# Kernel optimization log

Measured on AMD Instinct MI355X. Metric: run time of the kernel, lower is better.

## Reference

```python
import jax, jax.numpy as jnp
import numpy as np

THRESH = 0.3  # ternary threshold on |W|/mean(|W|)

def ternary_quantize(W):
    # scale = mean(|W|) clamped; q in {-1,0,+1} * scale
    scale = jnp.maximum(jnp.mean(jnp.abs(W)), 1e-8)
    ws = W / scale
    q = jnp.where(ws > THRESH, 1.0, jnp.where(ws < -THRESH, -1.0, 0.0))
    return q * scale

def quantize_activations(y):
    # per-token (last-dim) max-abs int8-style fake quant
    m = jnp.maximum(jnp.max(jnp.abs(y), axis=-1, keepdims=True), 1e-5)
    scale = 127.0 / m
    return jnp.round(jnp.clip(y * scale, -127.0, 127.0)) / scale

def setup_inputs() -> dict:
    key = jax.random.key(0)
    k1, k2, k3, k4, k5 = jax.random.split(key, 5)
    N, D_IN, D_OUT = 16384, 2048, 2048
    x = jax.random.normal(k1, (N, D_IN), dtype=jnp.float32)
    W = jax.random.normal(k2, (D_OUT, D_IN), dtype=jnp.float32) * 0.02
    b = jax.random.normal(k3, (D_OUT,), dtype=jnp.float32) * 0.02
    We = jax.random.normal(k4, (D_OUT, D_IN), dtype=jnp.float32) * 0.02
    be = jax.random.normal(k5, (D_OUT,), dtype=jnp.float32) * 0.02
    return {"x": x, "W": W, "b": b, "We": We, "be": be}

def reference(x, W, b, We, be):
    chain = jax.nn.relu(x @ ternary_quantize(W).T + b)  # [N, D_OUT]
    encoded = x @ We.T + be                              # [N, D_OUT]
    return quantize_activations(chain + encoded)
```

## Files before the change

kernel.cpp:

```cpp
#include <hip/hip_runtime.h>
#include <hip/hip_bf16.h>
#include <math.h>

typedef __bf16 bf16;
typedef __bf16 bf16x8 __attribute__((ext_vector_type(8)));
typedef float  f32x4  __attribute__((ext_vector_type(4)));
typedef unsigned int u32;

#define NROWS 16384
#define KDIM  2048
#define NCOLS 2048

#define OFF_XBF   0
#define OFF_Q     67108864
#define OFF_EBF   75497472
#define OFF_PART  83886080
#define OFF_SCALE 83894272

__device__ __forceinline__ void gload16(const bf16* g, bf16* l) {
    __builtin_amdgcn_global_load_lds(
        (const __attribute__((address_space(1))) u32*)g,
        (__attribute__((address_space(3))) u32*)l,
        16, 0, 0);
}

__device__ __forceinline__ void BAR() {
    asm volatile("" ::: "memory");
    __builtin_amdgcn_s_barrier();
    asm volatile("" ::: "memory");
}

__global__ void k_rowsum_absW(const float* __restrict__ W, float* __restrict__ partials) {
    int row = blockIdx.x;
    int t = threadIdx.x;
    const float4* wr = (const float4*)(W + (size_t)row * KDIM);
    float4 a = wr[t * 2];
    float4 b = wr[t * 2 + 1];
    float s = fabsf(a.x) + fabsf(a.y) + fabsf(a.z) + fabsf(a.w)
            + fabsf(b.x) + fabsf(b.y) + fabsf(b.z) + fabsf(b.w);
    __shared__ float red[256];
    red[t] = s; __syncthreads();
    for (int off = 128; off > 0; off >>= 1) {
        if (t < off) red[t] += red[t + off];
        __syncthreads();
    }
    if (t == 0) partials[row] = red[0];
}

__global__ void k_scale(const float* __restrict__ partials, float* __restrict__ scale) {
    int t = threadIdx.x;
    double s = 0.0;
    for (int i = t; i < 2048; i += 256) s += (double)partials[i];
    __shared__ double red[256];
    red[t] = s; __syncthreads();
    for (int off = 128; off > 0; off >>= 1) {
        if (t < off) red[t] += red[t + off];
        __syncthreads();
    }
    if (t == 0) {
        float m = (float)(red[0] / 4194304.0);
        scale[0] = fmaxf(m, 1e-8f);
    }
}

__global__ void k_quant(const float* __restrict__ W, const float* __restrict__ We,
                        const float* __restrict__ scale_p,
                        bf16* __restrict__ q, bf16* __restrict__ ebf) {
    float scale = scale_p[0];
    size_t base = ((size_t)blockIdx.x * 256 + threadIdx.x) * 8;
    float4 w0 = *(const float4*)(W + base);
    float4 w1 = *(const float4*)(W + base + 4);
    float4 e0 = *(const float4*)(We + base);
    float4 e1 = *(const float4*)(We + base + 4);
    float wv[8] = {w0.x, w0.y, w0.z, w0.w, w1.x, w1.y, w1.z, w1.w};
    float ev[8] = {e0.x, e0.y, e0.z, e0.w, e1.x, e1.y, e1.z, e1.w};
    bf16x8 qv, bv;
#pragma unroll
    for (int i = 0; i < 8; i++) {
        float ws = wv[i] / scale;
        float qq = ws > 0.3f ? 1.0f : (ws < -0.3f ? -1.0f : 0.0f);
        qv[i] = (bf16)qq;
        bv[i] = (bf16)ev[i];
    }
    *(bf16x8*)(q + base)   = qv;
    *(bf16x8*)(ebf + base) = bv;
}

__global__ void k_cvt_x(const float* __restrict__ x, bf16* __restrict__ xbf) {
    size_t base = ((size_t)blockIdx.x * 256 + threadIdx.x) * 8;
    float4 a = *(const float4*)(x + base);
    float4 c = *(const float4*)(x + base + 4);
    float v[8] = {a.x, a.y, a.z, a.w, c.x, c.y, c.z, c.w};
    bf16x8 o;
#pragma unroll
    for (int i = 0; i < 8; i++) o[i] = (bf16)v[i];
    *(bf16x8*)(xbf + base) = o;
}

#define BM 128
#define BN 128
#define BK 64
#define KSTEPS (KDIM / BK)
#define BUFE (BM * BK + 2 * BN * BK)

__global__ __launch_bounds__(512)
void k_gemm_dual(const bf16* __restrict__ X, const bf16* __restrict__ Q,
                 const bf16* __restrict__ E,
                 const float* __restrict__ b, const float* __restrict__ be,
                 const float* __restrict__ scale_p, float* __restrict__ Y)
{
    __shared__ bf16 lds[3][BUFE];

    int t    = threadIdx.x;
    int lane = t & 63;
    int w    = t >> 6;
    int wr   = w >> 2;
    int wc   = w & 3;

    int id   = blockIdx.x;
    int swz  = (id & 7) * 256 + (id >> 3);
    int bRow = swz >> 4;
    int bCol = swz & 15;

    const bf16* gA  = X + (size_t)(bRow * BM) * KDIM;
    const bf16* gB1 = Q + (size_t)(bCol * BN) * KDIM;
    const bf16* gB2 = E + (size_t)(bCol * BN) * KDIM;

    int row0 = t >> 3;
    int colsw = ((t & 7) * 8) ^ ((row0 & 7) << 3);

    f32x4 acc1[4][2], acc2[4][2];
#pragma unroll
    for (int m = 0; m < 4; m++)
#pragma unroll
        for (int n = 0; n < 2; n++) {
            acc1[m][n] = (f32x4){0.f, 0.f, 0.f, 0.f};
            acc2[m][n] = (f32x4){0.f, 0.f, 0.f, 0.f};
        }

    int lrow = lane & 15;
    int lk   = lane >> 4;

    auto STAGE = [&](int buf, int ks) {
        bf16* LA  = &lds[buf][0];
        bf16* LB1 = &lds[buf][BM * BK];
        bf16* LB2 = &lds[buf][BM * BK + BN * BK];
        size_t kof = (size_t)ks * BK + colsw;
        gload16(gA  + (size_t)row0 * KDIM + kof,        &LA [t * 8]);
        gload16(gA  + (size_t)(row0 + 64) * KDIM + kof, &LA [(512 + t) * 8]);
        gload16(gB1 + (size_t)row0 * KDIM + kof,        &LB1[t * 8]);
        gload16(gB1 + (size_t)(row0 + 64) * KDIM + kof, &LB1[(512 + t) * 8]);
        gload16(gB2 + (size_t)row0 * KDIM + kof,        &LB2[t * 8]);
        gload16(gB2 + (size_t)(row0 + 64) * KDIM + kof, &LB2[(512 + t) * 8]);
    };

    auto COMPUTE = [&](int buf) {
        const bf16* LA  = &lds[buf][0];
        const bf16* LB1 = &lds[buf][BM * BK];
        const bf16* LB2 = &lds[buf][BM * BK + BN * BK];
#pragma unroll
        for (int kk = 0; kk < 2; kk++) {
            int ko = kk * 32 + lk * 8;
            bf16x8 af[4], bq[2], beo[2];
#pragma unroll
            for (int m = 0; m < 4; m++) {
                int ar = wr * 64 + m * 16 + lrow;
                af[m] = *(const bf16x8*)&LA[ar * BK + (ko ^ ((ar & 7) << 3))];
            }
#pragma unroll
            for (int n = 0; n < 2; n++) {
                int br = wc * 32 + n * 16 + lrow;
                int sc = ko ^ ((br & 7) << 3);
                bq [n] = *(const bf16x8*)&LB1[br * BK + sc];
                beo[n] = *(const bf16x8*)&LB2[br * BK + sc];
            }
            __builtin_amdgcn_s_setprio(1);
#pragma unroll
            for (int m = 0; m < 4; m++)
#pragma unroll
                for (int n = 0; n < 2; n++) {
                    acc1[m][n] = __builtin_amdgcn_mfma_f32_16x16x32_bf16(af[m], bq [n], acc1[m][n], 0, 0, 0);
                    acc2[m][n] = __builtin_amdgcn_mfma_f32_16x16x32_bf16(af[m], beo[n], acc2[m][n], 0, 0, 0);
                }
            __builtin_amdgcn_s_setprio(0);
        }
    };

    STAGE(0, 0);
    STAGE(1, 1);

#pragma unroll 1
    for (int T = 0; T < KSTEPS - 2; ++T) {
        STAGE((T + 2) % 3, T + 2);
        asm volatile("s_waitcnt vmcnt(12)" ::: "memory");
        BAR();
        COMPUTE(T % 3);
        asm volatile("s_waitcnt lgkmcnt(0)" ::: "memory");
        BAR();
    }
    asm volatile("s_waitcnt vmcnt(6)" ::: "memory");
    BAR();
    COMPUTE((KSTEPS - 2) % 3);
    asm volatile("s_waitcnt lgkmcnt(0)" ::: "memory");
    BAR();
    asm volatile("s_waitcnt vmcnt(0)" ::: "memory");
    BAR();
    COMPUTE((KSTEPS - 1) % 3);

    float scale = scale_p[0];
#pragma unroll
    for (int m = 0; m < 4; m++) {
        int gr0 = bRow * BM + wr * 64 + m * 16 + (lane >> 4) * 4;
#pragma unroll
        for (int n = 0; n < 2; n++) {
            int gc = bCol * BN + wc * 32 + n * 16 + (lane & 15);
            float bj  = b[gc];
            float bej = be[gc];
#pragma unroll
            for (int v = 0; v < 4; v++) {
                float chain = fmaxf(acc1[m][n][v] * scale + bj, 0.0f);
                float y = chain + acc2[m][n][v] + bej;
                Y[(size_t)(gr0 + v) * NCOLS + gc] = y;
            }
        }
    }
}

__global__ void k_quant_rows(float* __restrict__ Y) {
    int row = blockIdx.x;
    int t = threadIdx.x;
    float4* yv = (float4*)(Y + (size_t)row * NCOLS);
    float4 a = yv[t];
    float4 c = yv[t + 256];
    float mx = fmaxf(fmaxf(fmaxf(fabsf(a.x), fabsf(a.y)), fmaxf(fabsf(a.z), fabsf(a.w))),
                     fmaxf(fmaxf(fabsf(c.x), fabsf(c.y)), fmaxf(fabsf(c.z), fabsf(c.w))));
    __shared__ float red[256];
    red[t] = mx; __syncthreads();
    for (int off = 128; off > 0; off >>= 1) {
        if (t < off) red[t] = fmaxf(red[t], red[t + off]);
        __syncthreads();
    }
    float m = fmaxf(red[0], 1e-5f);
    float qs = 127.0f / m;
    float4 oa, oc;
    oa.x = rintf(fminf(fmaxf(a.x * qs, -127.f), 127.f)) / qs;
    oa.y = rintf(fminf(fmaxf(a.y * qs, -127.f), 127.f)) / qs;
    oa.z = rintf(fminf(fmaxf(a.z * qs, -127.f), 127.f)) / qs;
    oa.w = rintf(fminf(fmaxf(a.w * qs, -127.f), 127.f)) / qs;
    oc.x = rintf(fminf(fmaxf(c.x * qs, -127.f), 127.f)) / qs;
    oc.y = rintf(fminf(fmaxf(c.y * qs, -127.f), 127.f)) / qs;
    oc.z = rintf(fminf(fmaxf(c.z * qs, -127.f), 127.f)) / qs;
    oc.w = rintf(fminf(fmaxf(c.w * qs, -127.f), 127.f)) / qs;
    yv[t] = oa;
    yv[t + 256] = oc;
}

extern "C" void kernel_launch(void* const* d_in, const int* in_sizes, int n_in,
                              void* d_out, int out_size, void* d_ws, size_t ws_size,
                              hipStream_t stream) {
    const float* x  = (const float*)d_in[0];
    const float* W  = (const float*)d_in[1];
    const float* b  = (const float*)d_in[2];
    const float* We = (const float*)d_in[3];
    const float* be = (const float*)d_in[4];
    float* out = (float*)d_out;

    char* ws = (char*)d_ws;
    bf16*  xbf      = (bf16*)(ws + OFF_XBF);
    bf16*  q        = (bf16*)(ws + OFF_Q);
    bf16*  ebf      = (bf16*)(ws + OFF_EBF);
    float* partials = (float*)(ws + OFF_PART);
    float* scale    = (float*)(ws + OFF_SCALE);

    k_rowsum_absW<<<2048, 256, 0, stream>>>(W, partials);
    k_scale<<<1, 256, 0, stream>>>(partials, scale);
    k_quant<<<2048, 256, 0, stream>>>(W, We, scale, q, ebf);
    k_cvt_x<<<16384, 256, 0, stream>>>(x, xbf);

    k_gemm_dual<<<(NROWS / BM) * (NCOLS / BN), 512, 0, stream>>>(xbf, q, ebf, b, be, scale, out);

    k_quant_rows<<<NROWS, 256, 0, stream>>>(out);
}
```

Baseline: 375.5 us.

## Interleave half-tile global staging with MFMA phases and drop block swizzle

Splits each K-step into two phases. Each phase reads LDS fragments, issues half of the next tile's global-to-LDS loads, synchronizes, then runs MFMAs, so load issue is spread across the compute instead of batched up front. It also replaces the XCD-aware block-index swizzle with a plain 2D grid mapping. The extra barriers per step add synchronization cost, and dropping the swizzle may hurt L2 locality across the chiplets.

```diff
diff --git a/kernel.cpp b/kernel.cpp
--- a/kernel.cpp
+++ b/kernel.cpp
@@ -101,7 +101,7 @@
 #define BN 128
 #define BK 64
 #define KSTEPS (KDIM / BK)
-#define BUFE (BM * BK + 2 * BN * BK)
+#define BUFE (3 * BM * BK)
 
 __global__ __launch_bounds__(512)
 void k_gemm_dual(const bf16* __restrict__ X, const bf16* __restrict__ Q,
@@ -117,10 +117,8 @@
     int wr   = w >> 2;
     int wc   = w & 3;
 
-    int id   = blockIdx.x;
-    int swz  = (id & 7) * 256 + (id >> 3);
-    int bRow = swz >> 4;
-    int bCol = swz & 15;
+    int bCol = blockIdx.x;
+    int bRow = blockIdx.y;
 
     const bf16* gA  = X + (size_t)(bRow * BM) * KDIM;
     const bf16* gB1 = Q + (size_t)(bCol * BN) * KDIM;
@@ -141,71 +139,81 @@
     int lrow = lane & 15;
     int lk   = lane >> 4;
 
-    auto STAGE = [&](int buf, int ks) {
-        bf16* LA  = &lds[buf][0];
-        bf16* LB1 = &lds[buf][BM * BK];
-        bf16* LB2 = &lds[buf][BM * BK + BN * BK];
+    auto STAGEH = [&](bf16* B, int ks, int h) {
         size_t kof = (size_t)ks * BK + colsw;
-        gload16(gA  + (size_t)row0 * KDIM + kof,        &LA [t * 8]);
-        gload16(gA  + (size_t)(row0 + 64) * KDIM + kof, &LA [(512 + t) * 8]);
-        gload16(gB1 + (size_t)row0 * KDIM + kof,        &LB1[t * 8]);
-        gload16(gB1 + (size_t)(row0 + 64) * KDIM + kof, &LB1[(512 + t) * 8]);
-        gload16(gB2 + (size_t)row0 * KDIM + kof,        &LB2[t * 8]);
-        gload16(gB2 + (size_t)(row0 + 64) * KDIM + kof, &LB2[(512 + t) * 8]);
+        int r   = row0 + h * 64;
+        int off = (h * 512 + t) * 8;
+        gload16(gA  + (size_t)r * KDIM + kof, B + off);
+        gload16(gB1 + (size_t)r * KDIM + kof, B + BM * BK + off);
+        gload16(gB2 + (size_t)r * KDIM + kof, B + 2 * BM * BK + off);
     };
 
-    auto COMPUTE = [&](int buf) {
-        const bf16* LA  = &lds[buf][0];
-        const bf16* LB1 = &lds[buf][BM * BK];
-        const bf16* LB2 = &lds[buf][BM * BK + BN * BK];
-#pragma unroll
-        for (int kk = 0; kk < 2; kk++) {
-            int ko = kk * 32 + lk * 8;
-            bf16x8 af[4], bq[2], beo[2];
-#pragma unroll
-            for (int m = 0; m < 4; m++) {
-                int ar = wr * 64 + m * 16 + lrow;
-                af[m] = *(const bf16x8*)&LA[ar * BK + (ko ^ ((ar & 7) << 3))];
+    auto PHASE = [&](const bf16* L, int kk, bf16* SB, int stile, int h, bool doStage) {
+        const bf16* LA  = L;
+        const bf16* LB1 = L + BM * BK;
+        const bf16* LB2 = L + 2 * BM * BK;
+        int ko = kk * 32 + lk * 8;
+        bf16x8 af[4], bq[2], beo[2];
+#pragma unroll
+        for (int m = 0; m < 4; m++) {
+            int ar = wr * 64 + m * 16 + lrow;
+            af[m] = *(const bf16x8*)&LA[ar * BK + (ko ^ ((ar & 7) << 3))];
+        }
+#pragma unroll
+        for (int n = 0; n < 2; n++) {
+            int br = wc * 32 + n * 16 + lrow;
+            int sc = ko ^ ((br & 7) << 3);
+            bq [n] = *(const bf16x8*)&LB1[br * BK + sc];
+            beo[n] = *(const bf16x8*)&LB2[br * BK + sc];
+        }
+        if (doStage) STAGEH(SB, stile, h);
+        BAR();
+        asm volatile("s_waitcnt lgkmcnt(0)" ::: "memory");
+        __builtin_amdgcn_sched_barrier(0);
+        __builtin_amdgcn_s_setprio(1);
+#pragma unroll
+        for (int m = 0; m < 4; m++)
+#pragma unroll
+            for (int n = 0; n < 2; n++) {
+                acc1[m][n] = __builtin_amdgcn_mfma_f32_16x16x32_bf16(af[m], bq [n], acc1[m][n], 0, 0, 0);
+                acc2[m][n] = __builtin_amdgcn_mfma_f32_16x16x32_bf16(af[m], beo[n], acc2[m][n], 0, 0, 0);
             }
-#pragma unroll
-            for (int n = 0; n < 2; n++) {
-                int br = wc * 32 + n * 16 + lrow;
-                int sc = ko ^ ((br & 7) << 3);
-                bq [n] = *(const bf16x8*)&LB1[br * BK + sc];
-                beo[n] = *(const bf16x8*)&LB2[br * BK + sc];
-            }
-            __builtin_amdgcn_s_setprio(1);
-#pragma unroll
-            for (int m = 0; m < 4; m++)
-#pragma unroll
-                for (int n = 0; n < 2; n++) {
-                    acc1[m][n] = __builtin_amdgcn_mfma_f32_16x16x32_bf16(af[m], bq [n], acc1[m][n], 0, 0, 0);
-                    acc2[m][n] = __builtin_amdgcn_mfma_f32_16x16x32_bf16(af[m], beo[n], acc2[m][n], 0, 0, 0);
-                }
-            __builtin_amdgcn_s_setprio(0);
-        }
+        __builtin_amdgcn_s_setprio(0);
     };
 
-    STAGE(0, 0);
-    STAGE(1, 1);
-
+    STAGEH(&lds[0][0], 0, 0); STAGEH(&lds[0][0], 0, 1);
+    STAGEH(&lds[1][0], 1, 0); STAGEH(&lds[1][0], 1, 1);
+    asm volatile("s_waitcnt vmcnt(6)" ::: "memory");
+    BAR();
+
+    int cb = 0;
 #pragma unroll 1
     for (int T = 0; T < KSTEPS - 2; ++T) {
-        STAGE((T + 2) % 3, T + 2);
-        asm volatile("s_waitcnt vmcnt(12)" ::: "memory");
-        BAR();
-        COMPUTE(T % 3);
-        asm volatile("s_waitcnt lgkmcnt(0)" ::: "memory");
-        BAR();
-    }
-    asm volatile("s_waitcnt vmcnt(6)" ::: "memory");
-    BAR();
-    COMPUTE((KSTEPS - 2) % 3);
-    asm volatile("s_waitcnt lgkmcnt(0)" ::: "memory");
-    BAR();
-    asm volatile("s_waitcnt vmcnt(0)" ::: "memory");
-    BAR();
-    COMPUTE((KSTEPS - 1) % 3);
+        bf16* cur = &lds[cb][0];
+        int sb = cb + 2; if (sb >= 3) sb -= 3;
+        bf16* stg = &lds[sb][0];
+        PHASE(cur, 0, stg, T + 2, 0, true);
+        BAR();
+        PHASE(cur, 1, stg, T + 2, 1, true);
+        asm volatile("s_waitcnt vmcnt(6)" ::: "memory");
+        BAR();
+        ++cb; if (cb == 3) cb = 0;
+    }
+    {
+        bf16* cur = &lds[cb][0];
+        PHASE(cur, 0, nullptr, 0, 0, false);
+        BAR();
+        PHASE(cur, 1, nullptr, 0, 0, false);
+        asm volatile("s_waitcnt vmcnt(0)" ::: "memory");
+        BAR();
+        ++cb; if (cb == 3) cb = 0;
+    }
+    {
+        bf16* cur = &lds[cb][0];
+        PHASE(cur, 0, nullptr, 0, 0, false);
+        BAR();
+        PHASE(cur, 1, nullptr, 0, 0, false);
+    }
 
     float scale = scale_p[0];
 #pragma unroll
@@ -277,7 +285,8 @@
     k_quant<<<2048, 256, 0, stream>>>(W, We, scale, q, ebf);
     k_cvt_x<<<16384, 256, 0, stream>>>(x, xbf);
 
-    k_gemm_dual<<<(NROWS / BM) * (NCOLS / BN), 512, 0, stream>>>(xbf, q, ebf, b, be, scale, out);
+    dim3 g(NCOLS / BN, NROWS / BM);
+    k_gemm_dual<<<g, 512, 0, stream>>>(xbf, q, ebf, b, be, scale, out);
 
     k_quant_rows<<<NROWS, 256, 0, stream>>>(out);
 }
```

Result: faster. 350.6 us (-6.6%).
